# Optimization experiments

Hardware: AMD Instinct MI355X
Metric: run time of the kernel (lower is better)

The kernel has to match this reference:

```python
import jax, jax.numpy as jnp
import numpy as np

NUM_EMBEDDINGS = 1024
EMBEDDING_DIM = 128
COMMITMENT_COST = 0.25


def setup_inputs() -> dict:
    key = jax.random.key(0)
    k_in, k_cb = jax.random.split(key)
    inputs = jax.random.normal(k_in, (8, EMBEDDING_DIM, 16, 32, 32), dtype=jnp.float32)
    # torch init: uniform_(-1/num_embeddings, 1/num_embeddings)
    codebook = jax.random.uniform(
        k_cb, (NUM_EMBEDDINGS, EMBEDDING_DIM), dtype=jnp.float32,
        minval=-1.0 / NUM_EMBEDDINGS, maxval=1.0 / NUM_EMBEDDINGS)
    return {"inputs": inputs, "codebook": codebook}


def reference(inputs, codebook):
    # inputs: [B, C, D, H, W] with C == embedding_dim; codebook: [K, C]
    C = codebook.shape[1]
    flat = jnp.transpose(inputs, (0, 2, 3, 4, 1)).reshape(-1, C)  # [N, C]
    # squared L2 distances via the expanded form (matches torch code)
    distances = (jnp.sum(flat ** 2, axis=1, keepdims=True)
                 + jnp.sum(codebook ** 2, axis=1)
                 - 2.0 * flat @ codebook.T)  # [N, K]
    encoding_indices = jnp.argmin(distances, axis=1)  # [N]
    quantized = codebook[encoding_indices]  # [N, C]
    # NOTE: faithful to original bug — plain reshape back to channels-first
    # inputs.shape with no inverse permute (torch: quantized.view(inputs.shape))
    quantized = quantized.reshape(inputs.shape)
    e_latent_loss = jnp.mean((jax.lax.stop_gradient(quantized) - inputs) ** 2)
    q_latent_loss = jnp.mean((quantized - jax.lax.stop_gradient(inputs)) ** 2)
    loss = q_latent_loss + COMMITMENT_COST * e_latent_loss
    # straight-through estimator
    quantized_st = inputs + jax.lax.stop_gradient(quantized - inputs)
    return quantized_st, loss, encoding_indices
```

## Files before the change

### kernel.cpp

```cpp
#include <hip/hip_runtime.h>

typedef unsigned short u16;
typedef __attribute__((ext_vector_type(8))) short bf16x8;
typedef __attribute__((ext_vector_type(4))) float f32x4;

#define K_CB  1024
#define N_ROWS 131072
#define NUMEL (N_ROWS * 128)
#define TAU2 6.0e-4f
#define SMALLCAP 32768
#define FULLCAP  32768

#define GLOAD16(gp, lp) __builtin_amdgcn_global_load_lds( \
    (const __attribute__((address_space(1))) unsigned int*)(gp), \
    (__attribute__((address_space(3))) unsigned int*)(lp), 16, 0, 0)

__device__ __forceinline__ u16 f2bf(float x) {
    union { float f; unsigned int u; } a; a.f = x;
    unsigned int r = a.u + 0x7fffu + ((a.u >> 16) & 1u);
    return (u16)(r >> 16);
}

__global__ void prep_cb_kernel(const float* __restrict__ cb, float* __restrict__ bn,
                               u16* __restrict__ Bpl, int* __restrict__ cnts) {
    int k = blockIdx.x * 256 + threadIdx.x;
    if (blockIdx.x == 0 && threadIdx.x < 2) cnts[threadIdx.x] = 0;
    if (k >= K_CB) return;
    const float4* row4 = reinterpret_cast<const float4*>(cb) + k * 32;
    float s = 0.f;
    #pragma unroll
    for (int i = 0; i < 32; ++i) {
        float4 v = row4[i];
        s = fmaf(v.x, v.x, s); s = fmaf(v.y, v.y, s);
        s = fmaf(v.z, v.z, s); s = fmaf(v.w, v.w, s);
    }
    bn[k] = s;
    const float* rf = cb + k * 128;
    #pragma unroll
    for (int s8 = 0; s8 < 16; ++s8) {
        unsigned int hw[8];
        #pragma unroll
        for (int j = 0; j < 8; ++j) hw[j] = f2bf(rf[s8 * 8 + j]);
        uint4 H;
        H.x = hw[0] | (hw[1] << 16); H.y = hw[2] | (hw[3] << 16);
        H.z = hw[4] | (hw[5] << 16); H.w = hw[6] | (hw[7] << 16);
        *reinterpret_cast<uint4*>(&Bpl[((size_t)s8 * 1024 + k) * 8]) = H;
    }
}

__launch_bounds__(256, 3)
__global__ void gemm_fused_kernel(const float* __restrict__ in, const float* __restrict__ cb,
                                  const u16* __restrict__ Bpl, const float* __restrict__ bn,
                                  float* __restrict__ out_q, float* __restrict__ idx_out,
                                  uint2* __restrict__ smallL, int* __restrict__ fullL,
                                  int* __restrict__ cnts,
                                  float* __restrict__ deltas, float* __restrict__ partials) {
    __shared__ u16 A_s[16 * 64 * 8];
    __shared__ u16 Bb[2 * 4 * 256 * 8];
    __shared__ float bn_s[K_CB];
    __shared__ float red_s[4];

    const int tid = threadIdx.x;
    const int w = tid >> 6, lane = tid & 63, g4 = lane >> 4, l15 = lane & 15;
    const int blk = blockIdx.x, n0 = blk * 64;

    #pragma unroll
    for (int i = 0; i < 4; ++i) {
        const u16* g = Bpl + (size_t)(w * 1024 + i * 64 + lane) * 8;
        GLOAD16(g, &Bb[(w * 256 + i * 64) * 8]);
    }
    for (int i = tid; i < K_CB; i += 256) bn_s[i] = bn[i];

    {
        const int base = (n0 >> 14) * (128 * 16384) + (n0 & 16383);
        #pragma unroll
        for (int i = 0; i < 4; ++i) {
            int p = tid + i * 256;
            int n = p & 63, s = p >> 6;
            const float* g = in + base + (size_t)(s * 8) * 16384 + n;
            unsigned int pw[8];
            #pragma unroll
            for (int j = 0; j < 8; ++j) pw[j] = f2bf(g[(size_t)j * 16384]);
            uint4 H;
            H.x = pw[0] | (pw[1] << 16); H.y = pw[2] | (pw[3] << 16);
            H.z = pw[4] | (pw[5] << 16); H.w = pw[6] | (pw[7] << 16);
            *reinterpret_cast<uint4*>(&A_s[(s * 64 + n) * 8]) = H;
        }
    }
    __syncthreads();

    f32x4 acc[4][4];
    const f32x4 zz = {0.f, 0.f, 0.f, 0.f};
    #pragma unroll
    for (int mi = 0; mi < 4; ++mi)
        #pragma unroll
        for (int ni = 0; ni < 4; ++ni) acc[mi][ni] = zz;

    float b1[16], b2[16]; int i1[16];
    #pragma unroll
    for (int sl = 0; sl < 16; ++sl) { b1[sl] = 3.4e38f; b2[sl] = 3.4e38f; i1[sl] = 0; }

    #pragma unroll
    for (int t = 0; t < 16; ++t) {
        const int chunk = t >> 2, cc = t & 3, buf = t & 1;
        if (t < 15) {
            const int t2 = t + 1, chunk2 = t2 >> 2, cc2 = t2 & 3, nb = t2 & 1;
            #pragma unroll
            for (int i = 0; i < 4; ++i) {
                const u16* g = Bpl + (size_t)((cc2 * 4 + w) * 1024 + chunk2 * 256 + i * 64 + lane) * 8;
                GLOAD16(g, &Bb[((nb * 4 + w) * 256 + i * 64) * 8]);
            }
        }
        bf16x8 af[4], bfr[4];
        #pragma unroll
        for (int mi = 0; mi < 4; ++mi)
            af[mi] = *reinterpret_cast<const bf16x8*>(
                &A_s[((cc * 4 + g4) * 64 + mi * 16 + l15) * 8]);
        #pragma unroll
        for (int ni = 0; ni < 4; ++ni)
            bfr[ni] = *reinterpret_cast<const bf16x8*>(
                &Bb[((buf * 4 + g4) * 256 + w * 64 + ni * 16 + l15) * 8]);
        #pragma unroll
        for (int mi = 0; mi < 4; ++mi)
            #pragma unroll
            for (int ni = 0; ni < 4; ++ni)
                acc[mi][ni] = __builtin_amdgcn_mfma_f32_16x16x32_bf16(af[mi], bfr[ni], acc[mi][ni], 0, 0, 0);

        if (cc == 3) {
            const int cb0s = chunk * 256;
            #pragma unroll
            for (int mi = 0; mi < 4; ++mi) {
                #pragma unroll
                for (int ni = 0; ni < 4; ++ni) {
                    int n = cb0s + w * 64 + ni * 16 + l15;
                    float bnv = bn_s[n];
                    #pragma unroll
                    for (int r = 0; r < 4; ++r) {
                        float s = fmaf(-2.0f, acc[mi][ni][r], bnv);
                        int sl = mi * 4 + r;
                        if (s < b1[sl]) { b2[sl] = b1[sl]; b1[sl] = s; i1[sl] = n; }
                        else if (s < b2[sl]) b2[sl] = s;
                    }
                    acc[mi][ni] = zz;
                }
            }
        }
        __syncthreads();
    }

    float* m_b1   = (float*)Bb;
    float* m_b2   = m_b1 + 256;
    int*   m_i1   = (int*)(m_b2 + 256);
    int*   idx_s  = m_i1 + 256;
    float* gmin_s = (float*)(idx_s + 64);
    int*   flg_s  = (int*)(gmin_s + 64);
    int*   ccnt_s = flg_s + 64;
    int*   fb_s   = ccnt_s + 64;
    int*   cand_s = fb_s + 64;

    #pragma unroll
    for (int sl = 0; sl < 16; ++sl) {
        float v1 = b1[sl], v2 = b2[sl]; int ix = i1[sl];
        #pragma unroll
        for (int m = 1; m < 16; m <<= 1) {
            float o1 = __shfl_xor(v1, m, 64);
            int   oi = __shfl_xor(ix, m, 64);
            float o2 = __shfl_xor(v2, m, 64);
            if (o1 < v1 || (o1 == v1 && oi < ix)) { v2 = fminf(v1, o2); v1 = o1; ix = oi; }
            else v2 = fminf(v2, o1);
        }
        if (l15 == 0) {
            int mi = sl >> 2, r = sl & 3;
            int rl = mi * 16 + g4 * 4 + r;
            m_b1[w * 64 + rl] = v1; m_b2[w * 64 + rl] = v2; m_i1[w * 64 + rl] = ix;
        }
    }
    __syncthreads();
    if (tid < 64) {
        float v1 = m_b1[tid], v2 = m_b2[tid]; int ix = m_i1[tid];
        #pragma unroll
        for (int wv = 1; wv < 4; ++wv) {
            float o1 = m_b1[wv * 64 + tid], o2 = m_b2[wv * 64 + tid]; int oi = m_i1[wv * 64 + tid];
            if (o1 < v1 || (o1 == v1 && oi < ix)) { v2 = fminf(v1, o2); v1 = o1; ix = oi; }
            else v2 = fminf(v2, o1);
        }
        idx_s[tid] = ix;
        idx_out[n0 + tid] = (float)ix;
        deltas[n0 + tid] = 0.f;
        gmin_s[tid] = v1;
        flg_s[tid] = (v2 - v1 <= TAU2) ? 1 : 0;
        ccnt_s[tid] = 0;
        fb_s[tid] = 0;
    }
    __syncthreads();

    #pragma unroll
    for (int sl = 0; sl < 16; ++sl) {
        int mi = sl >> 2, r = sl & 3;
        int rl = mi * 16 + g4 * 4 + r;
        if (flg_s[rl]) {
            float g = gmin_s[rl];
            if (b1[sl] - g <= TAU2) {
                int p = atomicAdd(&ccnt_s[rl], 1);
                if (p < 4) cand_s[rl * 4 + p] = i1[sl]; else fb_s[rl] = 1;
            }
            if (b2[sl] - g <= TAU2) fb_s[rl] = 1;
        }
    }
    __syncthreads();
    if (tid < 64 && flg_s[tid]) {
        int nc = ccnt_s[tid];
        int row = n0 + tid;
        if (!fb_s[tid] && nc >= 2) {
            int p = atomicAdd(&cnts[0], 1);
            if (p < SMALLCAP) {
                unsigned long long key = (unsigned long long)row |
                                         ((unsigned long long)nc << 20);
                for (int j = 0; j < nc; ++j)
                    key |= (unsigned long long)(cand_s[tid * 4 + j] & 1023) << (24 + 10 * j);
                uint2 rec; rec.x = (unsigned)key; rec.y = (unsigned)(key >> 32);
                smallL[p] = rec;
            } else {
                int q = atomicAdd(&cnts[1], 1);
                if (q < FULLCAP) fullL[q] = row;
            }
        } else if (fb_s[tid]) {
            int q = atomicAdd(&cnts[1], 1);
            if (q < FULLCAP) fullL[q] = row;
        }
    }
    __syncthreads();

    float acc_l = 0.f;
    const float4* cb4 = reinterpret_cast<const float4*>(cb);
    const float4* in4 = reinterpret_cast<const float4*>(in);
    float4* out4 = reinterpret_cast<float4*>(out_q);
    #pragma unroll
    for (int i = 0; i < 8; ++i) {
        int idx = tid + i * 256;
        int row = idx >> 5;
        int c4 = idx & 31;
        int kq = idx_s[row];
        float4 q = cb4[kq * 32 + c4];
        float4 x = in4[(size_t)(n0 + row) * 32 + c4];
        float4 d, o;
        d.x = q.x - x.x; d.y = q.y - x.y; d.z = q.z - x.z; d.w = q.w - x.w;
        o.x = x.x + d.x; o.y = x.y + d.y; o.z = x.z + d.z; o.w = x.w + d.w;
        out4[(size_t)(n0 + row) * 32 + c4] = o;
        acc_l += d.x * d.x; acc_l += d.y * d.y; acc_l += d.z * d.z; acc_l += d.w * d.w;
    }
    #pragma unroll
    for (int m = 1; m < 64; m <<= 1) acc_l += __shfl_xor(acc_l, m, 64);
    if ((tid & 63) == 0) red_s[tid >> 6] = acc_l;
    __syncthreads();
    if (tid == 0) partials[blk] = red_s[0] + red_s[1] + red_s[2] + red_s[3];
}

__device__ __forceinline__ void patch_row(const float* __restrict__ in,
                                          const float* __restrict__ cb,
                                          float* __restrict__ idx_out,
                                          float* __restrict__ out_q,
                                          float* __restrict__ deltas,
                                          int row, int k_new, int lane) {
    int k_old = (int)idx_out[row];
    if (k_new == k_old) return;
    if (lane == 0) idx_out[row] = (float)k_new;
    float dd = 0.f;
    if (lane < 32) {
        const float4* in4 = reinterpret_cast<const float4*>(in);
        const float4* cb4 = reinterpret_cast<const float4*>(cb);
        float4* out4 = reinterpret_cast<float4*>(out_q);
        float4 x = in4[(size_t)row * 32 + lane];
        float4 qn = cb4[(size_t)k_new * 32 + lane];
        float4 qo = cb4[(size_t)k_old * 32 + lane];
        float4 dn, dl, o;
        dn.x = qn.x - x.x; dn.y = qn.y - x.y; dn.z = qn.z - x.z; dn.w = qn.w - x.w;
        o.x = x.x + dn.x; o.y = x.y + dn.y; o.z = x.z + dn.z; o.w = x.w + dn.w;
        out4[(size_t)row * 32 + lane] = o;
        dl.x = qo.x - x.x; dl.y = qo.y - x.y; dl.z = qo.z - x.z; dl.w = qo.w - x.w;
        dd = dn.x * dn.x + dn.y * dn.y + dn.z * dn.z + dn.w * dn.w
           - (dl.x * dl.x + dl.y * dl.y + dl.z * dl.z + dl.w * dl.w);
    }
    #pragma unroll
    for (int m = 1; m < 64; m <<= 1) dd += __shfl_xor(dd, m, 64);
    if (lane == 0) deltas[row] = dd;
}

__global__ void small_rescore_kernel(const float* __restrict__ in, const float* __restrict__ cb,
                                     const float* __restrict__ bn, const uint2* __restrict__ recs,
                                     const int* __restrict__ cnts, float* __restrict__ idx_out,
                                     float* __restrict__ out_q, float* __restrict__ deltas) {
    __shared__ float xls[4][128];
    const int tid = threadIdx.x, wv = tid >> 6, lane = tid & 63;
    int ns = cnts[0]; if (ns > SMALLCAP) ns = SMALLCAP;
    float* xl = xls[wv];
    for (int f = blockIdx.x * 4 + wv; f < ns; f += gridDim.x * 4) {
        uint2 rc = recs[f];
        unsigned long long key = ((unsigned long long)rc.y << 32) | (unsigned long long)rc.x;
        int row = (int)(key & 131071ull);
        int nc = (int)((key >> 20) & 7ull);
        int ck = (lane < 4) ? (int)((key >> (24 + 10 * lane)) & 1023ull) : 0;
        const float* bp = in + (size_t)(row >> 14) * 2097152 + (row & 16383);
        xl[2 * lane]     = bp[(size_t)(2 * lane) * 16384];
        xl[2 * lane + 1] = bp[(size_t)(2 * lane + 1) * 16384];
        asm volatile("s_waitcnt vmcnt(0) lgkmcnt(0)" ::: "memory");
        float xn = 0.f;
        for (int c = 0; c < 128; ++c) { float v = xl[c]; xn = fmaf(v, v, xn); }
        float s = 3.4e38f; int kk = 0x7fffffff;
        if (lane < nc) {
            const float4* cr = reinterpret_cast<const float4*>(cb + (size_t)ck * 128);
            float dot = 0.f;
            #pragma unroll
            for (int c4 = 0; c4 < 32; ++c4) {
                float4 bv = cr[c4];
                float4 xv = *reinterpret_cast<const float4*>(&xl[c4 * 4]);
                dot = fmaf(xv.x, bv.x, dot); dot = fmaf(xv.y, bv.y, dot);
                dot = fmaf(xv.z, bv.z, dot); dot = fmaf(xv.w, bv.w, dot);
            }
            float t1 = xn + bn[ck];
            s = fmaf(-2.0f, dot, t1);
            kk = ck;
        }
        #pragma unroll
        for (int m = 1; m < 4; m <<= 1) {
            float os = __shfl_xor(s, m, 64);
            int ok = __shfl_xor(kk, m, 64);
            if (os < s || (os == s && ok < kk)) { s = os; kk = ok; }
        }
        int k_new = __shfl(kk, 0, 64);
        patch_row(in, cb, idx_out, out_q, deltas, row, k_new, lane);
    }
}

__global__ void full_rescore_kernel(const float* __restrict__ in, const float* __restrict__ cb,
                                    const float* __restrict__ bn, const int* __restrict__ fullL,
                                    const int* __restrict__ cnts, float* __restrict__ idx_out,
                                    float* __restrict__ out_q, float* __restrict__ deltas) {
    __shared__ float xls[4][128];
    const int tid = threadIdx.x, wv = tid >> 6, lane = tid & 63;
    int nf = cnts[1]; if (nf > FULLCAP) nf = FULLCAP;
    float* xl = xls[wv];
    for (int f = blockIdx.x * 4 + wv; f < nf; f += gridDim.x * 4) {
        int row = fullL[f];
        const float* bp = in + (size_t)(row >> 14) * 2097152 + (row & 16383);
        xl[2 * lane]     = bp[(size_t)(2 * lane) * 16384];
        xl[2 * lane + 1] = bp[(size_t)(2 * lane + 1) * 16384];
        asm volatile("s_waitcnt vmcnt(0) lgkmcnt(0)" ::: "memory");
        float xn = 0.f;
        for (int c = 0; c < 128; ++c) { float v = xl[c]; xn = fmaf(v, v, xn); }
        float best = 3.4e38f; int bi = 0x7fffffff;
        for (int j = 0; j < 16; ++j) {
            int k = j * 64 + lane;
            const float4* cr = reinterpret_cast<const float4*>(cb + (size_t)k * 128);
            float dot = 0.f;
            #pragma unroll
            for (int c4 = 0; c4 < 32; ++c4) {
                float4 bv = cr[c4];
                float4 xv = *reinterpret_cast<const float4*>(&xl[c4 * 4]);
                dot = fmaf(xv.x, bv.x, dot); dot = fmaf(xv.y, bv.y, dot);
                dot = fmaf(xv.z, bv.z, dot); dot = fmaf(xv.w, bv.w, dot);
            }
            float t1 = xn + bn[k];
            float s = fmaf(-2.0f, dot, t1);
            if (s < best || (s == best && k < bi)) { best = s; bi = k; }
        }
        #pragma unroll
        for (int m = 1; m < 64; m <<= 1) {
            float os = __shfl_xor(best, m, 64);
            int ok = __shfl_xor(bi, m, 64);
            if (os < best || (os == best && ok < bi)) { best = os; bi = ok; }
        }
        int k_new = __shfl(bi, 0, 64);
        patch_row(in, cb, idx_out, out_q, deltas, row, k_new, lane);
    }
}

__global__ void loss_stage1(const float* __restrict__ partials, const float* __restrict__ deltas,
                            float* __restrict__ part2) {
    __shared__ float red_s[4];
    const int blk = blockIdx.x, tid = threadIdx.x;
    float s = 0.f;
    const float* dp = deltas + blk * 2048;
    for (int i = tid; i < 2048; i += 256) s += dp[i];
    if (tid < 32) s += partials[blk * 32 + tid];
    #pragma unroll
    for (int m = 1; m < 64; m <<= 1) s += __shfl_xor(s, m, 64);
    if ((tid & 63) == 0) red_s[tid >> 6] = s;
    __syncthreads();
    if (tid == 0) part2[blk] = red_s[0] + red_s[1] + red_s[2] + red_s[3];
}

__global__ void loss_stage2(const float* __restrict__ part2, float* __restrict__ out_loss) {
    const int tid = threadIdx.x;
    float s = part2[tid];
    #pragma unroll
    for (int m = 1; m < 64; m <<= 1) s += __shfl_xor(s, m, 64);
    if (tid == 0) out_loss[0] = 1.25f * (s / (float)NUMEL);
}

extern "C" void kernel_launch(void* const* d_in, const int* in_sizes, int n_in,
                              void* d_out, int out_size, void* d_ws, size_t ws_size,
                              hipStream_t stream) {
    (void)in_sizes; (void)n_in; (void)out_size; (void)ws_size;
    const float* in = (const float*)d_in[0];
    const float* cb = (const float*)d_in[1];
    float* out = (float*)d_out;

    char* ws = (char*)d_ws;
    float* bn       = (float*)(ws + 0);
    u16*   Bpl      = (u16*)(ws + 4096);
    uint2* smallL   = (uint2*)(ws + 528384);
    int*   fullL    = (int*)(ws + 790528);
    float* deltas   = (float*)(ws + 921600);
    float* partials = (float*)(ws + 1445888);
    float* part2    = (float*)(ws + 1454080);
    int*   cnts     = (int*)(ws + 1454336);

    float* idxf = out + NUMEL + 1;

    prep_cb_kernel<<<4, 256, 0, stream>>>(cb, bn, Bpl, cnts);
    gemm_fused_kernel<<<2048, 256, 0, stream>>>(in, cb, Bpl, bn, out, idxf,
                                                smallL, fullL, cnts, deltas, partials);
    small_rescore_kernel<<<1024, 256, 0, stream>>>(in, cb, bn, smallL, cnts, idxf, out, deltas);
    full_rescore_kernel<<<256, 256, 0, stream>>>(in, cb, bn, fullL, cnts, idxf, out, deltas);
    loss_stage1<<<64, 256, 0, stream>>>(partials, deltas, part2);
    loss_stage2<<<1, 64, 0, stream>>>(part2, out + NUMEL);
}
```

Before: 308.4 us.

## Split codebook columns across eight waves and keep A fragments in registers

```diff
diff --git a/kernel.cpp b/kernel.cpp
--- a/kernel.cpp
+++ b/kernel.cpp
@@ -48,7 +48,7 @@
     }
 }
 
-__launch_bounds__(256, 3)
+__launch_bounds__(512, 6)
 __global__ void gemm_fused_kernel(const float* __restrict__ in, const float* __restrict__ cb,
                                   const u16* __restrict__ Bpl, const float* __restrict__ bn,
                                   float* __restrict__ out_q, float* __restrict__ idx_out,
@@ -57,25 +57,25 @@
                                   float* __restrict__ deltas, float* __restrict__ partials) {
     __shared__ u16 A_s[16 * 64 * 8];
     __shared__ u16 Bb[2 * 4 * 256 * 8];
-    __shared__ float bn_s[K_CB];
-    __shared__ float red_s[4];
+    __shared__ float red_s[8];
 
     const int tid = threadIdx.x;
     const int w = tid >> 6, lane = tid & 63, g4 = lane >> 4, l15 = lane & 15;
     const int blk = blockIdx.x, n0 = blk * 64;
 
     #pragma unroll
-    for (int i = 0; i < 4; ++i) {
-        const u16* g = Bpl + (size_t)(w * 1024 + i * 64 + lane) * 8;
-        GLOAD16(g, &Bb[(w * 256 + i * 64) * 8]);
-    }
-    for (int i = tid; i < K_CB; i += 256) bn_s[i] = bn[i];
+    for (int i = 0; i < 2; ++i) {
+        int j = i * 512 + tid;
+        int sl = j >> 8, r = j & 255;
+        const u16* g = Bpl + (size_t)(sl * 1024 + r) * 8;
+        GLOAD16(g, &Bb[(size_t)j * 8]);
+    }
 
     {
         const int base = (n0 >> 14) * (128 * 16384) + (n0 & 16383);
         #pragma unroll
-        for (int i = 0; i < 4; ++i) {
-            int p = tid + i * 256;
+        for (int i = 0; i < 2; ++i) {
+            int p = tid + i * 512;
             int n = p & 63, s = p >> 6;
             const float* g = in + base + (size_t)(s * 8) * 16384 + n;
             unsigned int pw[8];
@@ -89,12 +89,20 @@
     }
     __syncthreads();
 
-    f32x4 acc[4][4];
+    bf16x8 af_all[4][4];
+    #pragma unroll
+    for (int cc = 0; cc < 4; ++cc)
+        #pragma unroll
+        for (int mi = 0; mi < 4; ++mi)
+            af_all[cc][mi] = *reinterpret_cast<const bf16x8*>(
+                &A_s[((cc * 4 + g4) * 64 + mi * 16 + l15) * 8]);
+
+    f32x4 acc[4][2];
     const f32x4 zz = {0.f, 0.f, 0.f, 0.f};
     #pragma unroll
     for (int mi = 0; mi < 4; ++mi)
         #pragma unroll
-        for (int ni = 0; ni < 4; ++ni) acc[mi][ni] = zz;
+        for (int ni = 0; ni < 2; ++ni) acc[mi][ni] = zz;
 
     float b1[16], b2[16]; int i1[16];
     #pragma unroll
@@ -104,36 +112,33 @@
     for (int t = 0; t < 16; ++t) {
         const int chunk = t >> 2, cc = t & 3, buf = t & 1;
         if (t < 15) {
-            const int t2 = t + 1, chunk2 = t2 >> 2, cc2 = t2 & 3, nb = t2 & 1;
-            #pragma unroll
-            for (int i = 0; i < 4; ++i) {
-                const u16* g = Bpl + (size_t)((cc2 * 4 + w) * 1024 + chunk2 * 256 + i * 64 + lane) * 8;
-                GLOAD16(g, &Bb[((nb * 4 + w) * 256 + i * 64) * 8]);
-            }
-        }
-        bf16x8 af[4], bfr[4];
+            const int t2 = t + 1, ch2 = t2 >> 2, cc2 = t2 & 3, nb = t2 & 1;
+            #pragma unroll
+            for (int i = 0; i < 2; ++i) {
+                int j = i * 512 + tid;
+                int sl = j >> 8, r = j & 255;
+                const u16* g = Bpl + (size_t)((cc2 * 4 + sl) * 1024 + ch2 * 256 + r) * 8;
+                GLOAD16(g, &Bb[(size_t)(nb * 1024 + j) * 8]);
+            }
+        }
+        bf16x8 bfr[2];
+        #pragma unroll
+        for (int ni = 0; ni < 2; ++ni)
+            bfr[ni] = *reinterpret_cast<const bf16x8*>(
+                &Bb[((buf * 4 + g4) * 256 + w * 32 + ni * 16 + l15) * 8]);
         #pragma unroll
         for (int mi = 0; mi < 4; ++mi)
-            af[mi] = *reinterpret_cast<const bf16x8*>(
-                &A_s[((cc * 4 + g4) * 64 + mi * 16 + l15) * 8]);
-        #pragma unroll
-        for (int ni = 0; ni < 4; ++ni)
-            bfr[ni] = *reinterpret_cast<const bf16x8*>(
-                &Bb[((buf * 4 + g4) * 256 + w * 64 + ni * 16 + l15) * 8]);
-        #pragma unroll
-        for (int mi = 0; mi < 4; ++mi)
-            #pragma unroll
-            for (int ni = 0; ni < 4; ++ni)
-                acc[mi][ni] = __builtin_amdgcn_mfma_f32_16x16x32_bf16(af[mi], bfr[ni], acc[mi][ni], 0, 0, 0);
+            #pragma unroll
+            for (int ni = 0; ni < 2; ++ni)
+                acc[mi][ni] = __builtin_amdgcn_mfma_f32_16x16x32_bf16(af_all[cc][mi], bfr[ni], acc[mi][ni], 0, 0, 0);
 
         if (cc == 3) {
-            const int cb0s = chunk * 256;
-            #pragma unroll
-            for (int mi = 0; mi < 4; ++mi) {
+            #pragma unroll
+            for (int ni = 0; ni < 2; ++ni) {
+                int n = chunk * 256 + w * 32 + ni * 16 + l15;
+                float bnv = bn[n];
                 #pragma unroll
-                for (int ni = 0; ni < 4; ++ni) {
-                    int n = cb0s + w * 64 + ni * 16 + l15;
-                    float bnv = bn_s[n];
+                for (int mi = 0; mi < 4; ++mi) {
                     #pragma unroll
                     for (int r = 0; r < 4; ++r) {
                         float s = fmaf(-2.0f, acc[mi][ni][r], bnv);
@@ -149,9 +154,9 @@
     }
 
     float* m_b1   = (float*)Bb;
-    float* m_b2   = m_b1 + 256;
-    int*   m_i1   = (int*)(m_b2 + 256);
-    int*   idx_s  = m_i1 + 256;
+    float* m_b2   = m_b1 + 512;
+    int*   m_i1   = (int*)(m_b2 + 512);
+    int*   idx_s  = m_i1 + 512;
     float* gmin_s = (float*)(idx_s + 64);
     int*   flg_s  = (int*)(gmin_s + 64);
     int*   ccnt_s = flg_s + 64;
@@ -179,7 +184,7 @@
     if (tid < 64) {
         float v1 = m_b1[tid], v2 = m_b2[tid]; int ix = m_i1[tid];
         #pragma unroll
-        for (int wv = 1; wv < 4; ++wv) {
+        for (int wv = 1; wv < 8; ++wv) {
             float o1 = m_b1[wv * 64 + tid], o2 = m_b2[wv * 64 + tid]; int oi = m_i1[wv * 64 + tid];
             if (o1 < v1 || (o1 == v1 && oi < ix)) { v2 = fminf(v1, o2); v1 = o1; ix = oi; }
             else v2 = fminf(v2, o1);
@@ -236,8 +241,8 @@
     const float4* in4 = reinterpret_cast<const float4*>(in);
     float4* out4 = reinterpret_cast<float4*>(out_q);
     #pragma unroll
-    for (int i = 0; i < 8; ++i) {
-        int idx = tid + i * 256;
+    for (int i = 0; i < 4; ++i) {
+        int idx = tid + i * 512;
         int row = idx >> 5;
         int c4 = idx & 31;
         int kq = idx_s[row];
@@ -251,9 +256,14 @@
     }
     #pragma unroll
     for (int m = 1; m < 64; m <<= 1) acc_l += __shfl_xor(acc_l, m, 64);
-    if ((tid & 63) == 0) red_s[tid >> 6] = acc_l;
-    __syncthreads();
-    if (tid == 0) partials[blk] = red_s[0] + red_s[1] + red_s[2] + red_s[3];
+    if (lane == 0) red_s[w] = acc_l;
+    __syncthreads();
+    if (tid == 0) {
+        float s = 0.f;
+        #pragma unroll
+        for (int i = 0; i < 8; ++i) s += red_s[i];
+        partials[blk] = s;
+    }
 }
 
 __device__ __forceinline__ void patch_row(const float* __restrict__ in,
@@ -419,7 +429,7 @@
     float* idxf = out + NUMEL + 1;
 
     prep_cb_kernel<<<4, 256, 0, stream>>>(cb, bn, Bpl, cnts);
-    gemm_fused_kernel<<<2048, 256, 0, stream>>>(in, cb, Bpl, bn, out, idxf,
+    gemm_fused_kernel<<<2048, 512, 0, stream>>>(in, cb, Bpl, bn, out, idxf,
                                                 smallL, fullL, cnts, deltas, partials);
     small_rescore_kernel<<<1024, 256, 0, stream>>>(in, cb, bn, smallL, cnts, idxf, out, deltas);
     full_rescore_kernel<<<256, 256, 0, stream>>>(in, cb, bn, fullL, cnts, idxf, out, deltas);
```

Measured after the change: 1.034 ms (median of 2 runs). 3.35x slower.

## Hold A fragments in registers and reuse the A buffer for B double-buffering

Applied to the files above, without the earlier changes.

```diff
diff --git a/kernel.cpp b/kernel.cpp
--- a/kernel.cpp
+++ b/kernel.cpp
@@ -48,32 +48,23 @@
     }
 }
 
-__launch_bounds__(256, 3)
+__launch_bounds__(256, 4)
 __global__ void gemm_fused_kernel(const float* __restrict__ in, const float* __restrict__ cb,
                                   const u16* __restrict__ Bpl, const float* __restrict__ bn,
                                   float* __restrict__ out_q, float* __restrict__ idx_out,
                                   uint2* __restrict__ smallL, int* __restrict__ fullL,
                                   int* __restrict__ cnts,
                                   float* __restrict__ deltas, float* __restrict__ partials) {
-    __shared__ u16 A_s[16 * 64 * 8];
-    __shared__ u16 Bb[2 * 4 * 256 * 8];
+    __shared__ u16 B0[4 * 256 * 8];
+    __shared__ u16 AB1[4 * 256 * 8];
     __shared__ float bn_s[K_CB];
-    __shared__ float red_s[4];
 
     const int tid = threadIdx.x;
     const int w = tid >> 6, lane = tid & 63, g4 = lane >> 4, l15 = lane & 15;
     const int blk = blockIdx.x, n0 = blk * 64;
 
-    #pragma unroll
-    for (int i = 0; i < 4; ++i) {
-        const u16* g = Bpl + (size_t)(w * 1024 + i * 64 + lane) * 8;
-        GLOAD16(g, &Bb[(w * 256 + i * 64) * 8]);
-    }
-    for (int i = tid; i < K_CB; i += 256) bn_s[i] = bn[i];
-
     {
         const int base = (n0 >> 14) * (128 * 16384) + (n0 & 16383);
-        #pragma unroll
         for (int i = 0; i < 4; ++i) {
             int p = tid + i * 256;
             int n = p & 63, s = p >> 6;
@@ -84,9 +75,24 @@
             uint4 H;
             H.x = pw[0] | (pw[1] << 16); H.y = pw[2] | (pw[3] << 16);
             H.z = pw[4] | (pw[5] << 16); H.w = pw[6] | (pw[7] << 16);
-            *reinterpret_cast<uint4*>(&A_s[(s * 64 + n) * 8]) = H;
-        }
-    }
+            *reinterpret_cast<uint4*>(&AB1[(s * 64 + n) * 8]) = H;
+        }
+    }
+    for (int i = tid; i < K_CB; i += 256) bn_s[i] = bn[i];
+    #pragma unroll
+    for (int i = 0; i < 4; ++i) {
+        const u16* g = Bpl + (size_t)(w * 1024 + i * 64 + lane) * 8;
+        GLOAD16(g, &B0[(w * 256 + i * 64) * 8]);
+    }
+    __syncthreads();
+
+    bf16x8 af_all[4][4];
+    #pragma unroll
+    for (int cc = 0; cc < 4; ++cc)
+        #pragma unroll
+        for (int mi = 0; mi < 4; ++mi)
+            af_all[cc][mi] = *reinterpret_cast<const bf16x8*>(
+                &AB1[((cc * 4 + g4) * 64 + mi * 16 + l15) * 8]);
     __syncthreads();
 
     f32x4 acc[4][4];
@@ -100,55 +106,62 @@
     #pragma unroll
     for (int sl = 0; sl < 16; ++sl) { b1[sl] = 3.4e38f; b2[sl] = 3.4e38f; i1[sl] = 0; }
 
-    #pragma unroll
-    for (int t = 0; t < 16; ++t) {
-        const int chunk = t >> 2, cc = t & 3, buf = t & 1;
-        if (t < 15) {
-            const int t2 = t + 1, chunk2 = t2 >> 2, cc2 = t2 & 3, nb = t2 & 1;
-            #pragma unroll
-            for (int i = 0; i < 4; ++i) {
-                const u16* g = Bpl + (size_t)((cc2 * 4 + w) * 1024 + chunk2 * 256 + i * 64 + lane) * 8;
-                GLOAD16(g, &Bb[((nb * 4 + w) * 256 + i * 64) * 8]);
-            }
-        }
-        bf16x8 af[4], bfr[4];
-        #pragma unroll
-        for (int mi = 0; mi < 4; ++mi)
-            af[mi] = *reinterpret_cast<const bf16x8*>(
-                &A_s[((cc * 4 + g4) * 64 + mi * 16 + l15) * 8]);
-        #pragma unroll
-        for (int ni = 0; ni < 4; ++ni)
-            bfr[ni] = *reinterpret_cast<const bf16x8*>(
-                &Bb[((buf * 4 + g4) * 256 + w * 64 + ni * 16 + l15) * 8]);
-        #pragma unroll
-        for (int mi = 0; mi < 4; ++mi)
+    #pragma unroll 1
+    for (int chunk = 0; chunk < 4; ++chunk) {
+        #pragma unroll
+        for (int cc = 0; cc < 4; ++cc) {
+            if (!(cc == 3 && chunk == 3)) {
+                const int chn = chunk + (cc == 3 ? 1 : 0);
+                const int sln = (cc + 1) & 3;
+                u16* dst = ((cc + 1) & 1) ? AB1 : B0;
+                #pragma unroll
+                for (int i = 0; i < 4; ++i) {
+                    const u16* g = Bpl + (size_t)((sln * 4 + w) * 1024 + chn * 256 + i * 64 + lane) * 8;
+                    GLOAD16(g, &dst[(w * 256 + i * 64) * 8]);
+                }
+            }
+            const u16* src = (cc & 1) ? AB1 : B0;
+            bf16x8 bfr[4];
             #pragma unroll
             for (int ni = 0; ni < 4; ++ni)
-                acc[mi][ni] = __builtin_amdgcn_mfma_f32_16x16x32_bf16(af[mi], bfr[ni], acc[mi][ni], 0, 0, 0);
-
-        if (cc == 3) {
-            const int cb0s = chunk * 256;
+                bfr[ni] = *reinterpret_cast<const bf16x8*>(
+                    &src[(g4 * 256 + w * 64 + ni * 16 + l15) * 8]);
             #pragma unroll
-            for (int mi = 0; mi < 4; ++mi) {
+            for (int mi = 0; mi < 4; ++mi)
+                #pragma unroll
+                for (int ni = 0; ni < 4; ++ni)
+                    acc[mi][ni] = __builtin_amdgcn_mfma_f32_16x16x32_bf16(
+                        af_all[cc][mi], bfr[ni], acc[mi][ni], 0, 0, 0);
+
+            if (cc == 3) {
                 #pragma unroll
                 for (int ni = 0; ni < 4; ++ni) {
-                    int n = cb0s + w * 64 + ni * 16 + l15;
+                    int n = chunk * 256 + w * 64 + ni * 16 + l15;
                     float bnv = bn_s[n];
                     #pragma unroll
-                    for (int r = 0; r < 4; ++r) {
-                        float s = fmaf(-2.0f, acc[mi][ni][r], bnv);
-                        int sl = mi * 4 + r;
-                        if (s < b1[sl]) { b2[sl] = b1[sl]; b1[sl] = s; i1[sl] = n; }
-                        else if (s < b2[sl]) b2[sl] = s;
+                    for (int mi = 0; mi < 4; ++mi) {
+                        #pragma unroll
+                        for (int r = 0; r < 4; ++r) {
+                            float s = fmaf(-2.0f, acc[mi][ni][r], bnv);
+                            int sl = mi * 4 + r;
+                            float nb2 = fminf(fmaxf(s, b1[sl]), b2[sl]);
+                            bool lt = s < b1[sl];
+                            b1[sl] = lt ? s : b1[sl];
+                            i1[sl] = lt ? n : i1[sl];
+                            b2[sl] = nb2;
+                        }
+                        acc[mi][ni] = zz;
                     }
-                    acc[mi][ni] = zz;
                 }
             }
-        }
-        __syncthreads();
-    }
-
-    float* m_b1   = (float*)Bb;
+            asm volatile("s_waitcnt lgkmcnt(0)" ::: "memory");
+            asm volatile("s_waitcnt vmcnt(0)" ::: "memory");
+            __builtin_amdgcn_s_barrier();
+        }
+    }
+    __syncthreads();
+
+    float* m_b1   = (float*)B0;
     float* m_b2   = m_b1 + 256;
     int*   m_i1   = (int*)(m_b2 + 256);
     int*   idx_s  = m_i1 + 256;
@@ -157,6 +170,7 @@
     int*   ccnt_s = flg_s + 64;
     int*   fb_s   = ccnt_s + 64;
     int*   cand_s = fb_s + 64;
+    float* red_s  = (float*)(cand_s + 256);
 
     #pragma unroll
     for (int sl = 0; sl < 16; ++sl) {
@@ -251,7 +265,7 @@
     }
     #pragma unroll
     for (int m = 1; m < 64; m <<= 1) acc_l += __shfl_xor(acc_l, m, 64);
-    if ((tid & 63) == 0) red_s[tid >> 6] = acc_l;
+    if (lane == 0) red_s[w] = acc_l;
     __syncthreads();
     if (tid == 0) partials[blk] = red_s[0] + red_s[1] + red_s[2] + red_s[3];
 }
```

After: 442.7 us. 43.5% more time.

## Load codebook B fragments directly from global, drop LDS double buffer and barriers

Applied to the files above, without the earlier changes.

```diff
diff --git a/kernel.cpp b/kernel.cpp
--- a/kernel.cpp
+++ b/kernel.cpp
@@ -10,10 +10,6 @@
 #define TAU2 6.0e-4f
 #define SMALLCAP 32768
 #define FULLCAP  32768
-
-#define GLOAD16(gp, lp) __builtin_amdgcn_global_load_lds( \
-    (const __attribute__((address_space(1))) unsigned int*)(gp), \
-    (__attribute__((address_space(3))) unsigned int*)(lp), 16, 0, 0)
 
 __device__ __forceinline__ u16 f2bf(float x) {
     union { float f; unsigned int u; } a; a.f = x;
@@ -56,24 +52,24 @@
                                   int* __restrict__ cnts,
                                   float* __restrict__ deltas, float* __restrict__ partials) {
     __shared__ u16 A_s[16 * 64 * 8];
-    __shared__ u16 Bb[2 * 4 * 256 * 8];
     __shared__ float bn_s[K_CB];
+    __shared__ float m_b1s[4 * 64];
+    __shared__ float m_b2s[4 * 64];
+    __shared__ int   m_i1s[4 * 64];
+    __shared__ int   idx_s[64];
+    __shared__ float gmin_s[64];
+    __shared__ int   flg_s[64];
+    __shared__ int   ccnt_s[64];
+    __shared__ int   fb_s[64];
+    __shared__ int   cand_s[64 * 4];
     __shared__ float red_s[4];
 
     const int tid = threadIdx.x;
     const int w = tid >> 6, lane = tid & 63, g4 = lane >> 4, l15 = lane & 15;
     const int blk = blockIdx.x, n0 = blk * 64;
 
-    #pragma unroll
-    for (int i = 0; i < 4; ++i) {
-        const u16* g = Bpl + (size_t)(w * 1024 + i * 64 + lane) * 8;
-        GLOAD16(g, &Bb[(w * 256 + i * 64) * 8]);
-    }
-    for (int i = tid; i < K_CB; i += 256) bn_s[i] = bn[i];
-
     {
         const int base = (n0 >> 14) * (128 * 16384) + (n0 & 16383);
-        #pragma unroll
         for (int i = 0; i < 4; ++i) {
             int p = tid + i * 256;
             int n = p & 63, s = p >> 6;
@@ -87,6 +83,7 @@
             *reinterpret_cast<uint4*>(&A_s[(s * 64 + n) * 8]) = H;
         }
     }
+    for (int i = tid; i < K_CB; i += 256) bn_s[i] = bn[i];
     __syncthreads();
 
     f32x4 acc[4][4];
@@ -102,61 +99,46 @@
 
     #pragma unroll
     for (int t = 0; t < 16; ++t) {
-        const int chunk = t >> 2, cc = t & 3, buf = t & 1;
-        if (t < 15) {
-            const int t2 = t + 1, chunk2 = t2 >> 2, cc2 = t2 & 3, nb = t2 & 1;
-            #pragma unroll
-            for (int i = 0; i < 4; ++i) {
-                const u16* g = Bpl + (size_t)((cc2 * 4 + w) * 1024 + chunk2 * 256 + i * 64 + lane) * 8;
-                GLOAD16(g, &Bb[((nb * 4 + w) * 256 + i * 64) * 8]);
-            }
-        }
-        bf16x8 af[4], bfr[4];
+        const int chunk = t >> 2, cc = t & 3;
+        bf16x8 bfr[4];
+        #pragma unroll
+        for (int ni = 0; ni < 4; ++ni)
+            bfr[ni] = *reinterpret_cast<const bf16x8*>(
+                &Bpl[(size_t)((cc * 4 + g4) * 1024 + chunk * 256 + w * 64 + ni * 16 + l15) * 8]);
+        bf16x8 af[4];
         #pragma unroll
         for (int mi = 0; mi < 4; ++mi)
             af[mi] = *reinterpret_cast<const bf16x8*>(
                 &A_s[((cc * 4 + g4) * 64 + mi * 16 + l15) * 8]);
         #pragma unroll
-        for (int ni = 0; ni < 4; ++ni)
-            bfr[ni] = *reinterpret_cast<const bf16x8*>(
-                &Bb[((buf * 4 + g4) * 256 + w * 64 + ni * 16 + l15) * 8]);
-        #pragma unroll
         for (int mi = 0; mi < 4; ++mi)
             #pragma unroll
             for (int ni = 0; ni < 4; ++ni)
-                acc[mi][ni] = __builtin_amdgcn_mfma_f32_16x16x32_bf16(af[mi], bfr[ni], acc[mi][ni], 0, 0, 0);
+                acc[mi][ni] = __builtin_amdgcn_mfma_f32_16x16x32_bf16(
+                    af[mi], bfr[ni], acc[mi][ni], 0, 0, 0);
 
         if (cc == 3) {
-            const int cb0s = chunk * 256;
             #pragma unroll
-            for (int mi = 0; mi < 4; ++mi) {
+            for (int ni = 0; ni < 4; ++ni) {
+                int n = chunk * 256 + w * 64 + ni * 16 + l15;
+                float bnv = bn_s[n];
                 #pragma unroll
-                for (int ni = 0; ni < 4; ++ni) {
-                    int n = cb0s + w * 64 + ni * 16 + l15;
-                    float bnv = bn_s[n];
+                for (int mi = 0; mi < 4; ++mi) {
                     #pragma unroll
                     for (int r = 0; r < 4; ++r) {
                         float s = fmaf(-2.0f, acc[mi][ni][r], bnv);
                         int sl = mi * 4 + r;
-                        if (s < b1[sl]) { b2[sl] = b1[sl]; b1[sl] = s; i1[sl] = n; }
-                        else if (s < b2[sl]) b2[sl] = s;
+                        float nb2 = fminf(fmaxf(s, b1[sl]), b2[sl]);
+                        bool lt = s < b1[sl];
+                        b1[sl] = lt ? s : b1[sl];
+                        i1[sl] = lt ? n : i1[sl];
+                        b2[sl] = nb2;
                     }
                     acc[mi][ni] = zz;
                 }
             }
         }
-        __syncthreads();
-    }
-
-    float* m_b1   = (float*)Bb;
-    float* m_b2   = m_b1 + 256;
-    int*   m_i1   = (int*)(m_b2 + 256);
-    int*   idx_s  = m_i1 + 256;
-    float* gmin_s = (float*)(idx_s + 64);
-    int*   flg_s  = (int*)(gmin_s + 64);
-    int*   ccnt_s = flg_s + 64;
-    int*   fb_s   = ccnt_s + 64;
-    int*   cand_s = fb_s + 64;
+    }
 
     #pragma unroll
     for (int sl = 0; sl < 16; ++sl) {
@@ -172,15 +154,15 @@
         if (l15 == 0) {
             int mi = sl >> 2, r = sl & 3;
             int rl = mi * 16 + g4 * 4 + r;
-            m_b1[w * 64 + rl] = v1; m_b2[w * 64 + rl] = v2; m_i1[w * 64 + rl] = ix;
+            m_b1s[w * 64 + rl] = v1; m_b2s[w * 64 + rl] = v2; m_i1s[w * 64 + rl] = ix;
         }
     }
     __syncthreads();
     if (tid < 64) {
-        float v1 = m_b1[tid], v2 = m_b2[tid]; int ix = m_i1[tid];
+        float v1 = m_b1s[tid], v2 = m_b2s[tid]; int ix = m_i1s[tid];
         #pragma unroll
         for (int wv = 1; wv < 4; ++wv) {
-            float o1 = m_b1[wv * 64 + tid], o2 = m_b2[wv * 64 + tid]; int oi = m_i1[wv * 64 + tid];
+            float o1 = m_b1s[wv * 64 + tid], o2 = m_b2s[wv * 64 + tid]; int oi = m_i1s[wv * 64 + tid];
             if (o1 < v1 || (o1 == v1 && oi < ix)) { v2 = fminf(v1, o2); v1 = o1; ix = oi; }
             else v2 = fminf(v2, o1);
         }
@@ -251,7 +233,7 @@
     }
     #pragma unroll
     for (int m = 1; m < 64; m <<= 1) acc_l += __shfl_xor(acc_l, m, 64);
-    if ((tid & 63) == 0) red_s[tid >> 6] = acc_l;
+    if (lane == 0) red_s[w] = acc_l;
     __syncthreads();
     if (tid == 0) partials[blk] = red_s[0] + red_s[1] + red_s[2] + red_s[3];
 }
```

Result: slower. 666.8 us (+116.2%).
